# Kernel tuning notes

Hardware: AMD Instinct MI355X
Metric: run time of the kernel (lower is better)

## Reference

```python
import jax, jax.numpy as jnp
import numpy as np
import math

SQRT_K = math.sqrt(64.0)


def setup_inputs() -> dict:
    key = jax.random.key(0)
    ks = jax.random.split(key, 4)
    B, S, D, KS, VS = 4, 4096, 128, 64, 64
    scale = 1.0 / math.sqrt(D)
    return {
        "inputs": jax.random.normal(ks[0], (B, S, D), dtype=jnp.float32),
        "Wq": jax.random.normal(ks[1], (D, KS), dtype=jnp.float32) * scale,
        "bq": jnp.zeros((KS,), dtype=jnp.float32),
        "Wk": jax.random.normal(ks[2], (D, KS), dtype=jnp.float32) * scale,
        "bk": jnp.zeros((KS,), dtype=jnp.float32),
        "Wv": jax.random.normal(ks[3], (D, VS), dtype=jnp.float32) * scale,
        "bv": jnp.zeros((VS,), dtype=jnp.float32),
    }


def reference(inputs, Wq, bq, Wk, bk, Wv, bv):
    # QKV projections: [B,S,D] @ [D,K] -> [B,S,K]
    queries = inputs @ Wq + bq
    keys = inputs @ Wk + bk
    values = inputs @ Wv + bv
    # logits: [B,S,S]
    logits = jnp.einsum("bqk,bsk->bqs", queries, keys)
    S = logits.shape[-1]
    row = jnp.arange(S)[:, None]
    col = jnp.arange(S)[None, :]
    causal_mask = jnp.where(col > row, -jnp.inf, 0.0).astype(logits.dtype)
    logits = logits + causal_mask  # broadcast over batch
    probs = jax.nn.softmax(logits / SQRT_K, axis=-1)
    read = jnp.einsum("bqs,bsv->bqv", probs, values)  # [B,S,V]
    return jnp.concatenate([inputs, read], axis=-1)  # [B,S,D+V]
```

## Files before the change

### kernel.cpp

```cpp
#include <hip/hip_runtime.h>

#define B_ 4
#define S_ 4096
#define D_ 128
#define MCONST 12.0f

typedef short short8 __attribute__((ext_vector_type(8)));
typedef float f32x4 __attribute__((ext_vector_type(4)));
typedef unsigned short us4 __attribute__((ext_vector_type(4)));

__device__ __forceinline__ unsigned short f2b(float f) {
    unsigned u = __builtin_bit_cast(unsigned, f);
    u += 0x7fffu + ((u >> 16) & 1u);
    return (unsigned short)(u >> 16);
}

__device__ __forceinline__ short8 gld16(const unsigned short* p) {
    short8 r;
    asm volatile("global_load_dwordx4 %0, %1, off" : "=v"(r) : "v"(p) : "memory");
    return r;
}

__global__ void wtrans_k(const float* __restrict__ Wq, const float* __restrict__ Wk,
                         const float* __restrict__ Wv, unsigned short* __restrict__ Wt) {
    int idx = blockIdx.x * 256 + threadIdx.x;
    int d = idx / 192;
    int c = idx % 192;
    const float* Wm = (c < 64) ? Wq : (c < 128) ? Wk : Wv;
    int cm = c & 63;
    float v = Wm[d * 64 + cm];
    if (c < 64) v *= 0.125f;
    Wt[c * 128 + d] = f2b(v);
}

__global__ __launch_bounds__(256) void proj_k(
    const float* __restrict__ inp, const unsigned short* __restrict__ Wt,
    const float* __restrict__ bq, const float* __restrict__ bk, const float* __restrict__ bv,
    unsigned short* __restrict__ Qb, unsigned short* __restrict__ Kb,
    unsigned short* __restrict__ Vt, float* __restrict__ out) {
    __shared__ unsigned short in_s[64 * 128];
    __shared__ unsigned short w_s[192 * 128];
    int tid = threadIdx.x;
    int b = blockIdx.x >> 6;
    int s0 = (blockIdx.x & 63) << 6;

    for (int r = 0; r < 4; ++r) {
        int u = r * 256 + tid;
        int s = u >> 4, seg = u & 15;
        const float* src = inp + ((size_t)(b * S_ + s0 + s) * D_ + seg * 8);
        float4 v0 = *(const float4*)src;
        float4 v1 = *(const float4*)(src + 4);
        float* dst = out + ((size_t)(b * S_ + s0 + s) * 192 + seg * 8);
        *(float4*)dst = v0;
        *(float4*)(dst + 4) = v1;
        unsigned short h[8] = {f2b(v0.x), f2b(v0.y), f2b(v0.z), f2b(v0.w),
                               f2b(v1.x), f2b(v1.y), f2b(v1.z), f2b(v1.w)};
        int phys = seg ^ (s & 7);
        *(uint4*)(&in_s[s * 128 + phys * 8]) = *(uint4*)h;
    }
    for (int r = 0; r < 12; ++r) {
        int u = r * 256 + tid;
        int c = u >> 4, seg = u & 15;
        uint4 w = *(const uint4*)(Wt + c * 128 + seg * 8);
        int phys = seg ^ (c & 7);
        *(uint4*)(&w_s[c * 128 + phys * 8]) = w;
    }
    __syncthreads();

    int lane = tid & 63, wid = tid >> 6;
    int lo = lane & 15, hi = lane >> 4;
    f32x4 acc[4][3];
    for (int i = 0; i < 4; ++i)
        for (int j = 0; j < 3; ++j) acc[i][j] = (f32x4)0.f;

    for (int kk = 0; kk < 4; ++kk) {
        int unit = kk * 4 + hi;
        short8 a[4], bf[3];
        for (int rt = 0; rt < 4; ++rt) {
            int s = rt * 16 + lo;
            a[rt] = *(const short8*)(&in_s[s * 128 + (unit ^ (s & 7)) * 8]);
        }
        for (int j = 0; j < 3; ++j) {
            int c = (wid * 3 + j) * 16 + lo;
            bf[j] = *(const short8*)(&w_s[c * 128 + (unit ^ (c & 7)) * 8]);
        }
        for (int rt = 0; rt < 4; ++rt)
            for (int j = 0; j < 3; ++j)
                acc[rt][j] = __builtin_amdgcn_mfma_f32_16x16x32_bf16(a[rt], bf[j], acc[rt][j], 0, 0, 0);
    }

    for (int j = 0; j < 3; ++j) {
        int c = (wid * 3 + j) * 16 + lo;
        float bias = (c < 64) ? bq[c] * 0.125f : (c < 128) ? bk[c - 64] : bv[c - 128];
        for (int rt = 0; rt < 4; ++rt) {
            int sbase = s0 + rt * 16 + hi * 4;
            if (c < 128) {
                unsigned short* dst = (c < 64) ? Qb : Kb;
                int cc = c & 63;
                for (int r = 0; r < 4; ++r)
                    dst[(size_t)(b * S_ + sbase + r) * 64 + cc] = f2b(acc[rt][j][r] + bias);
            } else {
                int dv = c - 128;
                us4 h;
                for (int r = 0; r < 4; ++r) h[r] = f2b(acc[rt][j][r] + bias);
                *(us4*)(&Vt[(size_t)(b * 64 + dv) * S_ + sbase]) = h;
            }
        }
    }
}

__global__ __launch_bounds__(512, 2) void attn_k(
    const unsigned short* __restrict__ Qb, const unsigned short* __restrict__ Kb,
    const unsigned short* __restrict__ Vt, float* __restrict__ out,
    float* __restrict__ Op, float* __restrict__ Lp, int nh) {
    __shared__ __align__(16) unsigned char smem[51200];
    __shared__ float lbuf[8][16];
    unsigned short* kbuf = (unsigned short*)smem;
    unsigned short* vbuf = kbuf + 8192;
    unsigned short* pb   = kbuf + 16384;
    float* obuf = (float*)smem;

    int tid = threadIdx.x;
    int bid = blockIdx.x;
    int b = bid & 3;
    int u = bid >> 2;
    int t = 63 - u / nh;
    int h = u % nh;
    int lane = tid & 63, w = tid >> 6;
    int qsub = w & 3, kseg = w >> 2;
    int lo = lane & 15, hi = lane >> 4;
    int q0 = t * 64 + qsub * 16;
    int n_blk = t + 1;
    int nsup = (n_blk + 1) >> 1;
    int half = (nsup + nh - 1) / nh;
    int p0 = h * half;
    int pend = min(nsup, p0 + half);
    unsigned short* pls = pb + w * 1152;

    int srow = (tid >> 2) & 63;
    int sseg = (tid & 3) * 2;
    int sh = tid >> 8;
    int sdk = sh * 4096 + srow * 64;
    int sp0 = (sseg ^ (srow & 7)) * 8;
    int sp1 = ((sseg + 1) ^ (srow & 7)) * 8;
    const unsigned short* kgrow = Kb + ((size_t)b * S_ + srow) * 64 + sseg * 8;
    const unsigned short* vgrow = Vt + ((size_t)(b * 64 + srow)) * S_ + sseg * 8;

    short8 gk0, gk1, gv0, gv1;

    short8 qf0, qf1;
    {
        const unsigned short* qp = Qb + ((size_t)b * S_ + q0 + lo) * 64 + hi * 8;
        qf0 = *(const short8*)(qp);
        qf1 = *(const short8*)(qp + 32);
    }

    f32x4 o[4];
    for (int i = 0; i < 4; ++i) o[i] = (f32x4)0.f;
    f32x4 l4 = (f32x4)0.f;

    {
        int cc = 2 * p0 + sh;
        if (cc > 63) cc = 63;
        gk0 = gld16(kgrow + (size_t)cc * 4096);
        gk1 = gld16(kgrow + (size_t)cc * 4096 + 8);
        gv0 = gld16(vgrow + (size_t)cc * 64);
        gv1 = gld16(vgrow + (size_t)cc * 64 + 8);
        asm volatile("s_waitcnt vmcnt(0)" ::: "memory");
        __builtin_amdgcn_sched_barrier(0);
        *(short8*)(kbuf + sdk + sp0) = gk0;
        *(short8*)(kbuf + sdk + sp1) = gk1;
        *(short8*)(vbuf + sdk + sp0) = gv0;
        *(short8*)(vbuf + sdk + sp1) = gv1;
    }
    __syncthreads();

    for (int p = p0; p < pend; ++p) {
        bool more = (p + 1 < pend);
        if (more) {
            int cI = 2 * (p + 1) + sh;
            gk0 = gld16(kgrow + (size_t)cI * 4096);
            gk1 = gld16(kgrow + (size_t)cI * 4096 + 8);
            gv0 = gld16(vgrow + (size_t)cI * 64);
            gv1 = gld16(vgrow + (size_t)cI * 64 + 8);
        }
        int c = 2 * p + kseg;
        if (c < n_blk) {
            int kv0 = c << 6;
            int hb = kseg * 4096;
            f32x4 sc[4];
#pragma unroll
            for (int kvt = 0; kvt < 4; ++kvt) {
                const unsigned short* kp = kbuf + hb + (kvt * 16 + lo) * 64;
                short8 kf0 = *(const short8*)(kp + (hi ^ (lo & 7)) * 8);
                short8 kf1 = *(const short8*)(kp + ((hi + 4) ^ (lo & 7)) * 8);
                sc[kvt] = (f32x4)0.f;
                sc[kvt] = __builtin_amdgcn_mfma_f32_16x16x32_bf16(qf0, kf0, sc[kvt], 0, 0, 0);
                sc[kvt] = __builtin_amdgcn_mfma_f32_16x16x32_bf16(qf1, kf1, sc[kvt], 0, 0, 0);
            }
            bool diag = (kv0 + 63 > q0);
#pragma unroll
            for (int kvt = 0; kvt < 4; ++kvt)
#pragma unroll
                for (int r = 0; r < 4; ++r) {
                    float s = sc[kvt][r];
                    if (diag) {
                        int kvg = kv0 + kvt * 16 + lo;
                        int qg = q0 + hi * 4 + r;
                        if (kvg > qg) s = -3e38f;
                    }
                    float p2 = (s > -1e37f) ? __expf(s - MCONST) : 0.f;
                    l4[r] += p2;
                    pls[(hi * 4 + r) * 72 + kvt * 16 + lo] = f2b(p2);
                }
            short8 pa0 = *(const short8*)(&pls[lo * 72 + hi * 8]);
            short8 pa1 = *(const short8*)(&pls[lo * 72 + 32 + hi * 8]);
#pragma unroll
            for (int d = 0; d < 4; ++d) {
                const unsigned short* vp = vbuf + hb + (d * 16 + lo) * 64;
                short8 vf0 = *(const short8*)(vp + (hi ^ (lo & 7)) * 8);
                short8 vf1 = *(const short8*)(vp + ((hi + 4) ^ (lo & 7)) * 8);
                o[d] = __builtin_amdgcn_mfma_f32_16x16x32_bf16(pa0, vf0, o[d], 0, 0, 0);
                o[d] = __builtin_amdgcn_mfma_f32_16x16x32_bf16(pa1, vf1, o[d], 0, 0, 0);
            }
        }
        __syncthreads();
        if (more) {
            asm volatile("s_waitcnt vmcnt(0)" ::: "memory");
            __builtin_amdgcn_sched_barrier(0);
            *(short8*)(kbuf + sdk + sp0) = gk0;
            *(short8*)(kbuf + sdk + sp1) = gk1;
            *(short8*)(vbuf + sdk + sp0) = gv0;
            *(short8*)(vbuf + sdk + sp1) = gv1;
        }
        __syncthreads();
    }

    for (int off = 1; off < 16; off <<= 1)
        for (int r = 0; r < 4; ++r) l4[r] += __shfl_xor(l4[r], off);

    __syncthreads();

    if (lo == 0) {
        for (int r = 0; r < 4; ++r)
            lbuf[w][hi * 4 + r] = l4[r];
    }
    {
        float* ob = obuf + w * 1088;
        for (int d = 0; d < 4; ++d)
            for (int r = 0; r < 4; ++r)
                ob[(hi * 4 + r) * 68 + d * 16 + lo] = o[d][r];
    }
    __syncthreads();

    {
        int row = tid >> 3;
        int dv0 = (tid & 7) * 8;
        int mq = row & 15, ms = row >> 4;
        float L = lbuf[ms][mq] + lbuf[ms + 4][mq];
        const float* o0 = obuf + ms * 1088 + mq * 68 + dv0;
        const float* o1 = obuf + (ms + 4) * 1088 + mq * 68 + dv0;
        float4 x0 = *(const float4*)o0, y0 = *(const float4*)o1;
        float4 x1 = *(const float4*)(o0 + 4), y1 = *(const float4*)(o1 + 4);
        if (nh > 1) {
            int pblk = (t * nh + h) * 4 + b;
            float* pp = Op + (size_t)pblk * 4096 + row * 64 + dv0;
            float4 r0 = {x0.x + y0.x, x0.y + y0.y, x0.z + y0.z, x0.w + y0.w};
            float4 r1 = {x1.x + y1.x, x1.y + y1.y, x1.z + y1.z, x1.w + y1.w};
            *(float4*)pp = r0;
            *(float4*)(pp + 4) = r1;
            if ((tid & 7) == 0) Lp[pblk * 64 + row] = L;
        } else {
            float inv = 1.f / L;
            float4 r0 = {(x0.x + y0.x) * inv, (x0.y + y0.y) * inv,
                         (x0.z + y0.z) * inv, (x0.w + y0.w) * inv};
            float4 r1 = {(x1.x + y1.x) * inv, (x1.y + y1.y) * inv,
                         (x1.z + y1.z) * inv, (x1.w + y1.w) * inv};
            float* op = out + ((size_t)(b * S_ + t * 64 + row)) * 192 + 128 + dv0;
            *(float4*)op = r0;
            *(float4*)(op + 4) = r1;
        }
    }
}

__global__ __launch_bounds__(256) void merge_k(const float* __restrict__ Op,
                                               const float* __restrict__ Lp,
                                               float* __restrict__ out, int nh) {
    int g = blockIdx.x * 256 + threadIdx.x;
    int rg = g >> 4;
    int dv = (g & 15) * 4;
    int b = rg >> 12, q = rg & 4095;
    int t = q >> 6, row = q & 63;
    float L = 0.f;
    float4 a = {0.f, 0.f, 0.f, 0.f};
    for (int h = 0; h < nh; ++h) {
        int pblk = (t * nh + h) * 4 + b;
        L += Lp[pblk * 64 + row];
        float4 c = *(const float4*)(Op + (size_t)pblk * 4096 + row * 64 + dv);
        a.x += c.x; a.y += c.y; a.z += c.z; a.w += c.w;
    }
    float inv = 1.f / L;
    float4 r = {a.x * inv, a.y * inv, a.z * inv, a.w * inv};
    *(float4*)(&out[(size_t)rg * 192 + 128 + dv]) = r;
}

extern "C" void kernel_launch(void* const* d_in, const int* in_sizes, int n_in,
                              void* d_out, int out_size, void* d_ws, size_t ws_size,
                              hipStream_t stream) {
    const float* inp = (const float*)d_in[0];
    const float* Wq  = (const float*)d_in[1];
    const float* bq  = (const float*)d_in[2];
    const float* Wk  = (const float*)d_in[3];
    const float* bk  = (const float*)d_in[4];
    const float* Wv  = (const float*)d_in[5];
    const float* bv  = (const float*)d_in[6];
    float* out = (float*)d_out;

    char* ws = (char*)d_ws;
    unsigned short* Wt = (unsigned short*)ws;
    unsigned short* Qb = (unsigned short*)(ws + 49152);
    unsigned short* Kb = (unsigned short*)(ws + 49152 + 2097152);
    unsigned short* Vt = (unsigned short*)(ws + 49152 + 2 * 2097152);
    size_t opOff = 49152 + 3 * 2097152;
    float* Op = (float*)(ws + opOff);
    int nh = 1;
    if (ws_size >= opOff + (size_t)1024 * 4096 * 4 + 1024 * 64 * 4) nh = 4;
    else if (ws_size >= opOff + (size_t)512 * 4096 * 4 + 512 * 64 * 4) nh = 2;
    float* Lp = (float*)(ws + opOff + (size_t)(256 * nh) * 4096 * 4);

    wtrans_k<<<96, 256, 0, stream>>>(Wq, Wk, Wv, Wt);
    proj_k<<<256, 256, 0, stream>>>(inp, Wt, bq, bk, bv, Qb, Kb, Vt, out);
    if (nh > 1) {
        attn_k<<<256 * nh, 512, 0, stream>>>(Qb, Kb, Vt, out, Op, Lp, nh);
        merge_k<<<1024, 256, 0, stream>>>(Op, Lp, out, nh);
    } else {
        attn_k<<<256, 512, 0, stream>>>(Qb, Kb, Vt, out, Op, Lp, 1);
    }
}
```

Before: 53.43 us.

## Use 128-row query tiles per block with double-buffered 64-key tiles

Each attention block now covers 128 query rows, one 16-row slice per wave, instead of 64 rows split across two key segments. All eight waves share each 64-key K/V tile, so loaded keys are reused across twice as many queries. The tile sits in a double-buffered LDS slot, which drops one barrier per iteration. Per-wave outputs are written directly to global memory, removing the cross-wave LDS reduction. The trade-off is half as many blocks (fewer for CU occupancy) and a serial walk over key tiles, which lengthens each block's critical path.

Result: no change. 53.30 us (median of 2 runs) (-0.2%).

```diff
diff --git a/kernel.cpp b/kernel.cpp
--- a/kernel.cpp
+++ b/kernel.cpp
@@ -113,40 +113,34 @@
     const unsigned short* __restrict__ Qb, const unsigned short* __restrict__ Kb,
     const unsigned short* __restrict__ Vt, float* __restrict__ out,
     float* __restrict__ Op, float* __restrict__ Lp, int nh) {
-    __shared__ __align__(16) unsigned char smem[51200];
-    __shared__ float lbuf[8][16];
-    unsigned short* kbuf = (unsigned short*)smem;
-    unsigned short* vbuf = kbuf + 8192;
-    unsigned short* pb   = kbuf + 16384;
-    float* obuf = (float*)smem;
+    __shared__ __align__(16) unsigned short kbuf[2][64 * 64];
+    __shared__ __align__(16) unsigned short vbuf[2][64 * 64];
+    __shared__ unsigned short pb[8][16 * 72];
 
     int tid = threadIdx.x;
     int bid = blockIdx.x;
     int b = bid & 3;
     int u = bid >> 2;
-    int t = 63 - u / nh;
+    int t = 31 - u / nh;
     int h = u % nh;
     int lane = tid & 63, w = tid >> 6;
-    int qsub = w & 3, kseg = w >> 2;
     int lo = lane & 15, hi = lane >> 4;
-    int q0 = t * 64 + qsub * 16;
-    int n_blk = t + 1;
-    int nsup = (n_blk + 1) >> 1;
-    int half = (nsup + nh - 1) / nh;
-    int p0 = h * half;
-    int pend = min(nsup, p0 + half);
-    unsigned short* pls = pb + w * 1152;
-
-    int srow = (tid >> 2) & 63;
-    int sseg = (tid & 3) * 2;
-    int sh = tid >> 8;
-    int sdk = sh * 4096 + srow * 64;
-    int sp0 = (sseg ^ (srow & 7)) * 8;
-    int sp1 = ((sseg + 1) ^ (srow & 7)) * 8;
+    int q0 = t * 128 + w * 16;
+    int n_blk = 2 * t + 2;
+    int per = (n_blk + nh - 1) / nh;
+    int p0 = h * per;
+    int pend = min(n_blk, p0 + per);
+    int n_w = (q0 + 79) >> 6;
+    unsigned short* pls = &pb[w][0];
+
+    int srow = tid >> 3;
+    int sseg = tid & 7;
+    int sphys = (sseg ^ (srow & 7)) * 8;
+    int sdst = srow * 64 + sphys;
     const unsigned short* kgrow = Kb + ((size_t)b * S_ + srow) * 64 + sseg * 8;
     const unsigned short* vgrow = Vt + ((size_t)(b * 64 + srow)) * S_ + sseg * 8;
 
-    short8 gk0, gk1, gv0, gv1;
+    short8 gk, gv;
 
     short8 qf0, qf1;
     {
@@ -160,38 +154,28 @@
     f32x4 l4 = (f32x4)0.f;
 
     {
-        int cc = 2 * p0 + sh;
-        if (cc > 63) cc = 63;
-        gk0 = gld16(kgrow + (size_t)cc * 4096);
-        gk1 = gld16(kgrow + (size_t)cc * 4096 + 8);
-        gv0 = gld16(vgrow + (size_t)cc * 64);
-        gv1 = gld16(vgrow + (size_t)cc * 64 + 8);
+        gk = gld16(kgrow + (size_t)p0 * 4096);
+        gv = gld16(vgrow + (size_t)p0 * 64);
         asm volatile("s_waitcnt vmcnt(0)" ::: "memory");
         __builtin_amdgcn_sched_barrier(0);
-        *(short8*)(kbuf + sdk + sp0) = gk0;
-        *(short8*)(kbuf + sdk + sp1) = gk1;
-        *(short8*)(vbuf + sdk + sp0) = gv0;
-        *(short8*)(vbuf + sdk + sp1) = gv1;
+        *(short8*)(&kbuf[0][sdst]) = gk;
+        *(short8*)(&vbuf[0][sdst]) = gv;
     }
     __syncthreads();
 
     for (int p = p0; p < pend; ++p) {
+        int cur = (p - p0) & 1, nxt = cur ^ 1;
         bool more = (p + 1 < pend);
         if (more) {
-            int cI = 2 * (p + 1) + sh;
-            gk0 = gld16(kgrow + (size_t)cI * 4096);
-            gk1 = gld16(kgrow + (size_t)cI * 4096 + 8);
-            gv0 = gld16(vgrow + (size_t)cI * 64);
-            gv1 = gld16(vgrow + (size_t)cI * 64 + 8);
-        }
-        int c = 2 * p + kseg;
-        if (c < n_blk) {
-            int kv0 = c << 6;
-            int hb = kseg * 4096;
+            gk = gld16(kgrow + (size_t)(p + 1) * 4096);
+            gv = gld16(vgrow + (size_t)(p + 1) * 64);
+        }
+        if (p < n_w) {
+            int kv0 = p << 6;
             f32x4 sc[4];
 #pragma unroll
             for (int kvt = 0; kvt < 4; ++kvt) {
-                const unsigned short* kp = kbuf + hb + (kvt * 16 + lo) * 64;
+                const unsigned short* kp = &kbuf[cur][(kvt * 16 + lo) * 64];
                 short8 kf0 = *(const short8*)(kp + (hi ^ (lo & 7)) * 8);
                 short8 kf1 = *(const short8*)(kp + ((hi + 4) ^ (lo & 7)) * 8);
                 sc[kvt] = (f32x4)0.f;
@@ -217,21 +201,18 @@
             short8 pa1 = *(const short8*)(&pls[lo * 72 + 32 + hi * 8]);
 #pragma unroll
             for (int d = 0; d < 4; ++d) {
-                const unsigned short* vp = vbuf + hb + (d * 16 + lo) * 64;
+                const unsigned short* vp = &vbuf[cur][(d * 16 + lo) * 64];
                 short8 vf0 = *(const short8*)(vp + (hi ^ (lo & 7)) * 8);
                 short8 vf1 = *(const short8*)(vp + ((hi + 4) ^ (lo & 7)) * 8);
                 o[d] = __builtin_amdgcn_mfma_f32_16x16x32_bf16(pa0, vf0, o[d], 0, 0, 0);
                 o[d] = __builtin_amdgcn_mfma_f32_16x16x32_bf16(pa1, vf1, o[d], 0, 0, 0);
             }
         }
-        __syncthreads();
         if (more) {
             asm volatile("s_waitcnt vmcnt(0)" ::: "memory");
             __builtin_amdgcn_sched_barrier(0);
-            *(short8*)(kbuf + sdk + sp0) = gk0;
-            *(short8*)(kbuf + sdk + sp1) = gk1;
-            *(short8*)(vbuf + sdk + sp0) = gv0;
-            *(short8*)(vbuf + sdk + sp1) = gv1;
+            *(short8*)(&kbuf[nxt][sdst]) = gk;
+            *(short8*)(&vbuf[nxt][sdst]) = gv;
         }
         __syncthreads();
     }
@@ -239,46 +220,27 @@
     for (int off = 1; off < 16; off <<= 1)
         for (int r = 0; r < 4; ++r) l4[r] += __shfl_xor(l4[r], off);
 
-    __syncthreads();
-
-    if (lo == 0) {
-        for (int r = 0; r < 4; ++r)
-            lbuf[w][hi * 4 + r] = l4[r];
-    }
-    {
-        float* ob = obuf + w * 1088;
+    if (nh > 1) {
+        int pblk = (t * nh + h) * 4 + b;
+        float* pp = Op + (size_t)pblk * 8192 + (w * 16) * 64;
+#pragma unroll
         for (int d = 0; d < 4; ++d)
+#pragma unroll
             for (int r = 0; r < 4; ++r)
-                ob[(hi * 4 + r) * 68 + d * 16 + lo] = o[d][r];
-    }
-    __syncthreads();
-
-    {
-        int row = tid >> 3;
-        int dv0 = (tid & 7) * 8;
-        int mq = row & 15, ms = row >> 4;
-        float L = lbuf[ms][mq] + lbuf[ms + 4][mq];
-        const float* o0 = obuf + ms * 1088 + mq * 68 + dv0;
-        const float* o1 = obuf + (ms + 4) * 1088 + mq * 68 + dv0;
-        float4 x0 = *(const float4*)o0, y0 = *(const float4*)o1;
-        float4 x1 = *(const float4*)(o0 + 4), y1 = *(const float4*)(o1 + 4);
-        if (nh > 1) {
-            int pblk = (t * nh + h) * 4 + b;
-            float* pp = Op + (size_t)pblk * 4096 + row * 64 + dv0;
-            float4 r0 = {x0.x + y0.x, x0.y + y0.y, x0.z + y0.z, x0.w + y0.w};
-            float4 r1 = {x1.x + y1.x, x1.y + y1.y, x1.z + y1.z, x1.w + y1.w};
-            *(float4*)pp = r0;
-            *(float4*)(pp + 4) = r1;
-            if ((tid & 7) == 0) Lp[pblk * 64 + row] = L;
-        } else {
-            float inv = 1.f / L;
-            float4 r0 = {(x0.x + y0.x) * inv, (x0.y + y0.y) * inv,
-                         (x0.z + y0.z) * inv, (x0.w + y0.w) * inv};
-            float4 r1 = {(x1.x + y1.x) * inv, (x1.y + y1.y) * inv,
-                         (x1.z + y1.z) * inv, (x1.w + y1.w) * inv};
-            float* op = out + ((size_t)(b * S_ + t * 64 + row)) * 192 + 128 + dv0;
-            *(float4*)op = r0;
-            *(float4*)(op + 4) = r1;
+                pp[(hi * 4 + r) * 64 + d * 16 + lo] = o[d][r];
+        if (lo == 0) {
+#pragma unroll
+            for (int r = 0; r < 4; ++r)
+                Lp[pblk * 128 + w * 16 + hi * 4 + r] = l4[r];
+        }
+    } else {
+        float* op = out + ((size_t)(b * S_ + q0)) * 192 + 128;
+#pragma unroll
+        for (int r = 0; r < 4; ++r) {
+            float inv = 1.f / l4[r];
+#pragma unroll
+            for (int d = 0; d < 4; ++d)
+                op[(size_t)(hi * 4 + r) * 192 + d * 16 + lo] = o[d][r] * inv;
         }
     }
 }
@@ -290,13 +252,13 @@
     int rg = g >> 4;
     int dv = (g & 15) * 4;
     int b = rg >> 12, q = rg & 4095;
-    int t = q >> 6, row = q & 63;
+    int t = q >> 7, row = q & 127;
     float L = 0.f;
     float4 a = {0.f, 0.f, 0.f, 0.f};
     for (int h = 0; h < nh; ++h) {
         int pblk = (t * nh + h) * 4 + b;
-        L += Lp[pblk * 64 + row];
-        float4 c = *(const float4*)(Op + (size_t)pblk * 4096 + row * 64 + dv);
+        L += Lp[pblk * 128 + row];
+        float4 c = *(const float4*)(Op + (size_t)pblk * 8192 + row * 64 + dv);
         a.x += c.x; a.y += c.y; a.z += c.z; a.w += c.w;
     }
     float inv = 1.f / L;
@@ -324,16 +286,16 @@
     size_t opOff = 49152 + 3 * 2097152;
     float* Op = (float*)(ws + opOff);
     int nh = 1;
-    if (ws_size >= opOff + (size_t)1024 * 4096 * 4 + 1024 * 64 * 4) nh = 4;
-    else if (ws_size >= opOff + (size_t)512 * 4096 * 4 + 512 * 64 * 4) nh = 2;
-    float* Lp = (float*)(ws + opOff + (size_t)(256 * nh) * 4096 * 4);
+    if (ws_size >= opOff + (size_t)512 * 8192 * 4 + 512 * 128 * 4) nh = 4;
+    else if (ws_size >= opOff + (size_t)256 * 8192 * 4 + 256 * 128 * 4) nh = 2;
+    float* Lp = (float*)(ws + opOff + (size_t)(128 * nh) * 8192 * 4);
 
     wtrans_k<<<96, 256, 0, stream>>>(Wq, Wk, Wv, Wt);
     proj_k<<<256, 256, 0, stream>>>(inp, Wt, bq, bk, bv, Qb, Kb, Vt, out);
     if (nh > 1) {
-        attn_k<<<256 * nh, 512, 0, stream>>>(Qb, Kb, Vt, out, Op, Lp, nh);
+        attn_k<<<128 * nh, 512, 0, stream>>>(Qb, Kb, Vt, out, Op, Lp, nh);
         merge_k<<<1024, 256, 0, stream>>>(Op, Lp, out, nh);
     } else {
-        attn_k<<<256, 512, 0, stream>>>(Qb, Kb, Vt, out, Op, Lp, 1);
-    }
-}
+        attn_k<<<128, 512, 0, stream>>>(Qb, Kb, Vt, out, Op, Lp, 1);
+    }
+}
```
